# Kernel optimization log

Measured on AMD Instinct MI355X. Metric: run time of the kernel, lower is better.

The kernel has to match this reference:

```python
import jax, jax.numpy as jnp
import numpy as np

N_STATE = 1024
N_HEAD = 16
B = 2
S = 2048


def setup_inputs() -> dict:
    key = jax.random.key(0)
    ks = jax.random.split(key, 8)
    s = 0.02
    x = jax.random.normal(ks[0], (B, S, N_STATE), dtype=jnp.float32)
    # causal additive mask, as in Whisper: upper triangle = -inf
    mask = jnp.where(jnp.triu(jnp.ones((S, S), dtype=bool), k=1), -jnp.inf, 0.0).astype(jnp.float32)
    Wq = jax.random.normal(ks[1], (N_STATE, N_STATE), dtype=jnp.float32) * s
    bq = jax.random.normal(ks[2], (N_STATE,), dtype=jnp.float32) * s
    Wk = jax.random.normal(ks[3], (N_STATE, N_STATE), dtype=jnp.float32) * s
    Wv = jax.random.normal(ks[4], (N_STATE, N_STATE), dtype=jnp.float32) * s
    bv = jax.random.normal(ks[5], (N_STATE,), dtype=jnp.float32) * s
    Wo = jax.random.normal(ks[6], (N_STATE, N_STATE), dtype=jnp.float32) * s
    bo = jax.random.normal(ks[7], (N_STATE,), dtype=jnp.float32) * s
    return {"x": x, "mask": mask, "Wq": Wq, "bq": bq, "Wk": Wk,
            "Wv": Wv, "bv": bv, "Wo": Wo, "bo": bo}


def reference(x, mask, Wq, bq, Wk, Wv, bv, Wo, bo):
    Bb, S_, D = x.shape
    H = N_HEAD
    hd = D // H
    scale = hd ** (-0.25)  # scale split across q and k, as in the source
    q = x @ Wq.T + bq              # [B,S,D]
    k = x @ Wk.T                   # key has no bias
    v = x @ Wv.T + bv
    # [B,S,D] -> [B,H,S,hd]
    q = q.reshape(Bb, S_, H, hd).transpose(0, 2, 1, 3) * scale
    k = k.reshape(Bb, S_, H, hd).transpose(0, 2, 1, 3) * scale
    v = v.reshape(Bb, S_, H, hd).transpose(0, 2, 1, 3)
    qk = jnp.einsum('bhsd,bhtd->bhst', q, k) + mask[:S_, :S_]
    w = jax.nn.softmax(qk, axis=-1).astype(q.dtype)
    out = jnp.einsum('bhst,bhtd->bhsd', w, v)
    out = out.transpose(0, 2, 1, 3).reshape(Bb, S_, D)
    return out @ Wo.T + bo
```

## Files before the change

kernel.cpp:

```cpp
#include <hip/hip_runtime.h>
#include <hip/hip_bf16.h>
#include <cmath>

typedef __bf16 bf16;
typedef __bf16 bf16x8 __attribute__((ext_vector_type(8)));
typedef __bf16 bf16x4 __attribute__((ext_vector_type(4)));
typedef float f32x4 __attribute__((ext_vector_type(4)));

#define QS 0.18033688f

__device__ __forceinline__ void load16_to_lds(const void* g, void* l) {
    __builtin_amdgcn_global_load_lds(
        (const __attribute__((address_space(1))) unsigned int*)g,
        (__attribute__((address_space(3))) unsigned int*)l, 16, 0, 0);
}

__global__ __launch_bounds__(256) void convert_kernel(
    const float* __restrict__ x,  const float* __restrict__ wq,
    const float* __restrict__ wk, const float* __restrict__ wv,
    const float* __restrict__ wo, bf16* __restrict__ dst)
{
    const size_t M1 = 1024ull * 1024ull, M4 = 4ull * M1;
    size_t i0 = ((size_t)blockIdx.x * 256 + threadIdx.x) * 8;
    const float* s;
    size_t off;
    float sc = 1.f;
    if      (i0 < M4)        { s = x;  off = i0; }
    else if (i0 < M4 + M1)   { s = wq; off = i0 - M4; sc = QS; }
    else if (i0 < M4 + 2*M1) { s = wk; off = i0 - M4 - M1; }
    else if (i0 < M4 + 3*M1) { s = wv; off = i0 - M4 - 2*M1; }
    else                     { s = wo; off = i0 - M4 - 3*M1; }
    float4 a = *(const float4*)(s + off);
    float4 b = *(const float4*)(s + off + 4);
    bf16x8 r = { (bf16)(a.x*sc), (bf16)(a.y*sc), (bf16)(a.z*sc), (bf16)(a.w*sc),
                 (bf16)(b.x*sc), (bf16)(b.y*sc), (bf16)(b.z*sc), (bf16)(b.w*sc) };
    *(bf16x8*)(dst + i0) = r;
}

template<int BM, bool OUT_F32>
__device__ __forceinline__ void gemm_core(
    const bf16* __restrict__ A, const bf16* __restrict__ W,
    const float* __restrict__ bias, void* __restrict__ C,
    int mb, int nb, bool vt_out, float bias_scale)
{
    constexpr int IF = BM / 32;
    __shared__ __align__(16) bf16 As[BM * 32];
    __shared__ __align__(16) bf16 Bs[128 * 32];

    const int tid  = threadIdx.x;
    const int lane = tid & 63;
    const int wave = tid >> 6;
    const int wr   = (wave >> 1) * (BM / 2);
    const int wc   = (wave & 1) * 64;
    const int l15  = lane & 15;
    const int l4   = lane >> 4;
    const int swz  = (l4 ^ ((l15 >> 1) & 3)) * 8;

    f32x4 acc[IF][4] = {};

    for (int kt = 0; kt < 32; ++kt) {
#pragma unroll
        for (int it = 0; it < BM / 64; ++it) {
            int c = it * 256 + tid;
            int scol = ((c & 3) ^ ((c >> 3) & 3)) * 8;
            load16_to_lds(&A[(size_t)(mb * BM + (c >> 2)) * 1024 + kt * 32 + scol],
                          &As[(it * 256 + (tid & 192)) * 8]);
        }
#pragma unroll
        for (int it = 0; it < 2; ++it) {
            int c = it * 256 + tid;
            int scol = ((c & 3) ^ ((c >> 3) & 3)) * 8;
            load16_to_lds(&W[(size_t)(nb * 128 + (c >> 2)) * 1024 + kt * 32 + scol],
                          &Bs[(it * 256 + (tid & 192)) * 8]);
        }
        __syncthreads();
        bf16x8 af[IF], bfr[4];
#pragma unroll
        for (int i = 0; i < IF; ++i)
            af[i] = *(const bf16x8*)&As[(wr + i * 16 + l15) * 32 + swz];
#pragma unroll
        for (int j = 0; j < 4; ++j)
            bfr[j] = *(const bf16x8*)&Bs[(wc + j * 16 + l15) * 32 + swz];
#pragma unroll
        for (int i = 0; i < IF; ++i)
#pragma unroll
            for (int j = 0; j < 4; ++j)
                acc[i][j] = __builtin_amdgcn_mfma_f32_16x16x32_bf16(
                    af[i], bfr[j], acc[i][j], 0, 0, 0);
        __syncthreads();
    }

    if (!OUT_F32 && vt_out) {
#pragma unroll
        for (int j = 0; j < 4; ++j) {
            int col = nb * 128 + wc + j * 16 + l15;
            float bv = bias ? bias[col] : 0.f;
            int h = col >> 6, d = col & 63;
#pragma unroll
            for (int i = 0; i < IF; ++i) {
                int m0 = mb * BM + wr + i * 16 + l4 * 4;
                int b = m0 >> 11, s = m0 & 2047;
                bf16x4 pk = { (bf16)(acc[i][j][0] + bv), (bf16)(acc[i][j][1] + bv),
                              (bf16)(acc[i][j][2] + bv), (bf16)(acc[i][j][3] + bv) };
                *(bf16x4*)&((bf16*)C)[(size_t)((b * 16 + h) * 64 + d) * 2048 + s] = pk;
            }
        }
    } else {
#pragma unroll
        for (int j = 0; j < 4; ++j) {
            int col = nb * 128 + wc + j * 16 + l15;
            float bv = bias ? bias[col] * bias_scale : 0.f;
#pragma unroll
            for (int i = 0; i < IF; ++i) {
                int row0 = mb * BM + wr + i * 16 + l4 * 4;
#pragma unroll
                for (int r = 0; r < 4; ++r) {
                    float val = acc[i][j][r] + bv;
                    size_t idx = (size_t)(row0 + r) * 1024 + col;
                    if (OUT_F32) ((float*)C)[idx] = val;
                    else         ((bf16*)C)[idx]  = (bf16)val;
                }
            }
        }
    }
}

__global__ __launch_bounds__(256) void qkv_kernel(
    const bf16* __restrict__ xb,
    const bf16* __restrict__ wqb, const float* __restrict__ bq,
    const bf16* __restrict__ wkb,
    const bf16* __restrict__ wvb, const float* __restrict__ bv,
    bf16* __restrict__ q, bf16* __restrict__ k, bf16* __restrict__ vt)
{
    int mb = blockIdx.x;
    int nbg = blockIdx.y;
    int sel = nbg >> 3, nb = nbg & 7;
    const bf16* W = (sel == 0) ? wqb : ((sel == 1) ? wkb : wvb);
    const float* bias = (sel == 0) ? bq : ((sel == 2) ? bv : nullptr);
    bf16* C = (sel == 0) ? q : ((sel == 1) ? k : vt);
    gemm_core<128, false>(xb, W, bias, C, mb, nb, sel == 2,
                          sel == 0 ? QS : 1.f);
}

__global__ __launch_bounds__(256) void oproj_kernel(
    const bf16* __restrict__ ao, const bf16* __restrict__ wob,
    const float* __restrict__ bo, float* __restrict__ out)
{
    gemm_core<64, true>(ao, wob, bo, out, blockIdx.x, blockIdx.y, false, 1.f);
}

__global__ __launch_bounds__(256) void attn_kernel(
    const bf16* __restrict__ q, const bf16* __restrict__ k,
    const bf16* __restrict__ vt, bf16* __restrict__ o)
{
    __shared__ __align__(16) bf16 Ks[2][64 * 64];
    __shared__ __align__(16) bf16 Vs[2][64 * 64];
    __shared__ __align__(16) bf16 Ps[4][16 * 72];

    const int tid  = threadIdx.x;
    const int lane = tid & 63;
    const int wave = tid >> 6;
    const int l15  = lane & 15;
    const int l4   = lane >> 4;

    const int bh = blockIdx.x;
    const int pairIdx = blockIdx.y;
    const int b = bh >> 4, h = bh & 15;
    const int qts[2] = { pairIdx, 31 - pairIdx };

    auto stage = [&](int nt, int buf) {
#pragma unroll
        for (int it = 0; it < 2; ++it) {
            int c = it * 256 + tid;
            int scol = ((c & 7) ^ ((c >> 3) & 7)) * 8;
            load16_to_lds(&k[(size_t)(b * 2048 + nt * 64 + (c >> 3)) * 1024 + h * 64 + scol],
                          &Ks[buf][(it * 256 + (tid & 192)) * 8]);
            load16_to_lds(&vt[(size_t)(bh * 64 + (c >> 3)) * 2048 + nt * 64 + scol],
                          &Vs[buf][(it * 256 + (tid & 192)) * 8]);
        }
    };

    int b0 = 0;
    stage(0, 0);

    for (int seg = 0; seg < 2; ++seg) {
        const int qt = qts[seg];
        const int qg = qt * 64 + wave * 16 + l15;
        bf16x8 qf[2];
#pragma unroll
        for (int kk = 0; kk < 2; ++kk)
            qf[kk] = *(const bf16x8*)&q[(size_t)(b * 2048 + qg) * 1024 + h * 64 + kk * 32 + l4 * 8];

        f32x4 oacc[4] = {};
        float lsum = 0.f;

        const int n = qt + 1;
        for (int nt = 0; nt < n; ++nt) {
            __syncthreads();
            if (nt + 1 < n)      stage(nt + 1, b0 ^ 1);
            else if (seg == 0)   stage(0, b0 ^ 1);

            f32x4 s[4] = {};
#pragma unroll
            for (int kk = 0; kk < 2; ++kk) {
#pragma unroll
                for (int j = 0; j < 4; ++j) {
                    bf16x8 kf = *(const bf16x8*)&Ks[b0][(j * 16 + l15) * 64
                                    + (((kk * 4 + l4) ^ (l15 & 7)) * 8)];
                    s[j] = __builtin_amdgcn_mfma_f32_16x16x32_bf16(kf, qf[kk], s[j], 0, 0, 0);
                }
            }

            float pv[4][4];
            if (nt == qt) {
#pragma unroll
                for (int j = 0; j < 4; ++j)
#pragma unroll
                    for (int r = 0; r < 4; ++r) {
                        int kg = nt * 64 + j * 16 + l4 * 4 + r;
                        pv[j][r] = (kg > qg) ? 0.f : __builtin_amdgcn_exp2f(s[j][r]);
                    }
            } else {
#pragma unroll
                for (int j = 0; j < 4; ++j)
#pragma unroll
                    for (int r = 0; r < 4; ++r)
                        pv[j][r] = __builtin_amdgcn_exp2f(s[j][r]);
            }
#pragma unroll
            for (int j = 0; j < 4; ++j)
                lsum += (pv[j][0] + pv[j][1]) + (pv[j][2] + pv[j][3]);

#pragma unroll
            for (int j = 0; j < 4; ++j) {
                bf16x4 pk = { (bf16)pv[j][0], (bf16)pv[j][1], (bf16)pv[j][2], (bf16)pv[j][3] };
                *(bf16x4*)&Ps[wave][l15 * 72 + j * 16 + l4 * 4] = pk;
            }

#pragma unroll
            for (int kk = 0; kk < 2; ++kk) {
                bf16x8 pf = *(const bf16x8*)&Ps[wave][l15 * 72 + kk * 32 + l4 * 8];
#pragma unroll
                for (int f = 0; f < 4; ++f) {
                    bf16x8 vf = *(const bf16x8*)&Vs[b0][(f * 16 + l15) * 64
                                    + (((kk * 4 + l4) ^ (l15 & 7)) * 8)];
                    oacc[f] = __builtin_amdgcn_mfma_f32_16x16x32_bf16(pf, vf, oacc[f], 0, 0, 0);
                }
            }
            b0 ^= 1;
        }

        lsum += __shfl_xor(lsum, 16, 64);
        lsum += __shfl_xor(lsum, 32, 64);
        float rinv[4];
#pragma unroll
        for (int r = 0; r < 4; ++r) rinv[r] = 1.f / __shfl(lsum, l4 * 4 + r, 64);
#pragma unroll
        for (int f = 0; f < 4; ++f)
#pragma unroll
            for (int r = 0; r < 4; ++r)
                o[(size_t)(b * 2048 + qt * 64 + wave * 16 + l4 * 4 + r) * 1024 + h * 64 + f * 16 + l15]
                    = (bf16)(oacc[f][r] * rinv[r]);
    }
}

extern "C" void kernel_launch(void* const* d_in, const int* in_sizes, int n_in,
                              void* d_out, int out_size, void* d_ws, size_t ws_size,
                              hipStream_t stream)
{
    const float* x  = (const float*)d_in[0];
    const float* Wq = (const float*)d_in[2];
    const float* bq = (const float*)d_in[3];
    const float* Wk = (const float*)d_in[4];
    const float* Wv = (const float*)d_in[5];
    const float* bv = (const float*)d_in[6];
    const float* Wo = (const float*)d_in[7];
    const float* bo = (const float*)d_in[8];
    float* out = (float*)d_out;

    const size_t M1 = 1024ull * 1024ull, M4 = 4ull * M1;
    bf16* base = (bf16*)d_ws;
    bf16* xb  = base;
    bf16* wqb = base + M4;
    bf16* wkb = base + M4 + M1;
    bf16* wvb = base + M4 + 2 * M1;
    bf16* wob = base + M4 + 3 * M1;
    bf16* q   = base + 8 * M1;
    bf16* k   = base + 12 * M1;
    bf16* vt  = base + 16 * M1;
    bf16* ao  = xb;

    convert_kernel<<<4096, 256, 0, stream>>>(x, Wq, Wk, Wv, Wo, base);
    qkv_kernel<<<dim3(32, 24), 256, 0, stream>>>(xb, wqb, bq, wkb, wvb, bv, q, k, vt);
    attn_kernel<<<dim3(32, 16), 256, 0, stream>>>(q, k, vt, ao);
    oproj_kernel<<<dim3(64, 8), 256, 0, stream>>>(ao, wob, bo, out);
}
```

Before: 184.4 us.

## Process 128-row query tiles per attention block and enlarge o-proj GEMM tile

Each attention wave now handles two 16-row query sub-tiles (32 rows), so a block covers 128 query rows and reuses every staged K/V tile for twice as many queries. The grid shrinks to 8 balanced causal pairs per head, and waves skip key tiles that lie entirely above their rows. The output projection also switches to the 128-row GEMM tile with half the row blocks. This lowers K/V LDS staging and global traffic per query, at the cost of more registers, fewer blocks, and waves idling at barriers on skipped tiles.

```diff
diff --git a/kernel.cpp b/kernel.cpp
--- a/kernel.cpp
+++ b/kernel.cpp
@@ -146,7 +146,7 @@
     const bf16* __restrict__ ao, const bf16* __restrict__ wob,
     const float* __restrict__ bo, float* __restrict__ out)
 {
-    gemm_core<64, true>(ao, wob, bo, out, blockIdx.x, blockIdx.y, false, 1.f);
+    gemm_core<128, true>(ao, wob, bo, out, blockIdx.x, blockIdx.y, false, 1.f);
 }
 
 __global__ __launch_bounds__(256) void attn_kernel(
@@ -155,7 +155,7 @@
 {
     __shared__ __align__(16) bf16 Ks[2][64 * 64];
     __shared__ __align__(16) bf16 Vs[2][64 * 64];
-    __shared__ __align__(16) bf16 Ps[4][16 * 72];
+    __shared__ __align__(16) bf16 Ps[4][32 * 72];
 
     const int tid  = threadIdx.x;
     const int lane = tid & 63;
@@ -166,7 +166,7 @@
     const int bh = blockIdx.x;
     const int pairIdx = blockIdx.y;
     const int b = bh >> 4, h = bh & 15;
-    const int qts[2] = { pairIdx, 31 - pairIdx };
+    const int qts[2] = { pairIdx, 15 - pairIdx };
 
     auto stage = [&](int nt, int buf) {
 #pragma unroll
@@ -185,82 +185,99 @@
 
     for (int seg = 0; seg < 2; ++seg) {
         const int qt = qts[seg];
-        const int qg = qt * 64 + wave * 16 + l15;
-        bf16x8 qf[2];
-#pragma unroll
-        for (int kk = 0; kk < 2; ++kk)
-            qf[kk] = *(const bf16x8*)&q[(size_t)(b * 2048 + qg) * 1024 + h * 64 + kk * 32 + l4 * 8];
-
-        f32x4 oacc[4] = {};
-        float lsum = 0.f;
-
-        const int n = qt + 1;
+        const int qrow0 = qt * 128 + wave * 32;
+        bf16x8 qf[2][2];
+#pragma unroll
+        for (int qb = 0; qb < 2; ++qb)
+#pragma unroll
+            for (int kk = 0; kk < 2; ++kk)
+                qf[qb][kk] = *(const bf16x8*)&q[(size_t)(b * 2048 + qrow0 + qb * 16 + l15) * 1024
+                                               + h * 64 + kk * 32 + l4 * 8];
+
+        f32x4 oacc[2][4] = {};
+        float lsum[2] = { 0.f, 0.f };
+
+        const int n = 2 * qt + 2;
         for (int nt = 0; nt < n; ++nt) {
             __syncthreads();
             if (nt + 1 < n)      stage(nt + 1, b0 ^ 1);
             else if (seg == 0)   stage(0, b0 ^ 1);
 
-            f32x4 s[4] = {};
+            if (nt * 64 > qrow0 + 31) { b0 ^= 1; continue; }
+
+            f32x4 s[2][4] = {};
 #pragma unroll
             for (int kk = 0; kk < 2; ++kk) {
 #pragma unroll
                 for (int j = 0; j < 4; ++j) {
                     bf16x8 kf = *(const bf16x8*)&Ks[b0][(j * 16 + l15) * 64
                                     + (((kk * 4 + l4) ^ (l15 & 7)) * 8)];
-                    s[j] = __builtin_amdgcn_mfma_f32_16x16x32_bf16(kf, qf[kk], s[j], 0, 0, 0);
-                }
-            }
-
-            float pv[4][4];
-            if (nt == qt) {
+                    s[0][j] = __builtin_amdgcn_mfma_f32_16x16x32_bf16(kf, qf[0][kk], s[0][j], 0, 0, 0);
+                    s[1][j] = __builtin_amdgcn_mfma_f32_16x16x32_bf16(kf, qf[1][kk], s[1][j], 0, 0, 0);
+                }
+            }
+
+            const bool diag = (nt >= 2 * qt);
+#pragma unroll
+            for (int qb = 0; qb < 2; ++qb) {
+                float pv[4][4];
+                if (diag) {
+                    int qg = qrow0 + qb * 16 + l15;
+#pragma unroll
+                    for (int j = 0; j < 4; ++j)
+#pragma unroll
+                        for (int r = 0; r < 4; ++r) {
+                            int kg = nt * 64 + j * 16 + l4 * 4 + r;
+                            pv[j][r] = (kg > qg) ? 0.f : __builtin_amdgcn_exp2f(s[qb][j][r]);
+                        }
+                } else {
+#pragma unroll
+                    for (int j = 0; j < 4; ++j)
+#pragma unroll
+                        for (int r = 0; r < 4; ++r)
+                            pv[j][r] = __builtin_amdgcn_exp2f(s[qb][j][r]);
+                }
 #pragma unroll
                 for (int j = 0; j < 4; ++j)
-#pragma unroll
-                    for (int r = 0; r < 4; ++r) {
-                        int kg = nt * 64 + j * 16 + l4 * 4 + r;
-                        pv[j][r] = (kg > qg) ? 0.f : __builtin_amdgcn_exp2f(s[j][r]);
-                    }
-            } else {
-#pragma unroll
-                for (int j = 0; j < 4; ++j)
-#pragma unroll
-                    for (int r = 0; r < 4; ++r)
-                        pv[j][r] = __builtin_amdgcn_exp2f(s[j][r]);
-            }
-#pragma unroll
-            for (int j = 0; j < 4; ++j)
-                lsum += (pv[j][0] + pv[j][1]) + (pv[j][2] + pv[j][3]);
-
-#pragma unroll
-            for (int j = 0; j < 4; ++j) {
-                bf16x4 pk = { (bf16)pv[j][0], (bf16)pv[j][1], (bf16)pv[j][2], (bf16)pv[j][3] };
-                *(bf16x4*)&Ps[wave][l15 * 72 + j * 16 + l4 * 4] = pk;
+                    lsum[qb] += (pv[j][0] + pv[j][1]) + (pv[j][2] + pv[j][3]);
+
+#pragma unroll
+                for (int j = 0; j < 4; ++j) {
+                    bf16x4 pk = { (bf16)pv[j][0], (bf16)pv[j][1], (bf16)pv[j][2], (bf16)pv[j][3] };
+                    *(bf16x4*)&Ps[wave][(qb * 16 + l15) * 72 + j * 16 + l4 * 4] = pk;
+                }
             }
 
 #pragma unroll
             for (int kk = 0; kk < 2; ++kk) {
-                bf16x8 pf = *(const bf16x8*)&Ps[wave][l15 * 72 + kk * 32 + l4 * 8];
+                bf16x8 pf0 = *(const bf16x8*)&Ps[wave][l15 * 72 + kk * 32 + l4 * 8];
+                bf16x8 pf1 = *(const bf16x8*)&Ps[wave][(16 + l15) * 72 + kk * 32 + l4 * 8];
 #pragma unroll
                 for (int f = 0; f < 4; ++f) {
                     bf16x8 vf = *(const bf16x8*)&Vs[b0][(f * 16 + l15) * 64
                                     + (((kk * 4 + l4) ^ (l15 & 7)) * 8)];
-                    oacc[f] = __builtin_amdgcn_mfma_f32_16x16x32_bf16(pf, vf, oacc[f], 0, 0, 0);
+                    oacc[0][f] = __builtin_amdgcn_mfma_f32_16x16x32_bf16(pf0, vf, oacc[0][f], 0, 0, 0);
+                    oacc[1][f] = __builtin_amdgcn_mfma_f32_16x16x32_bf16(pf1, vf, oacc[1][f], 0, 0, 0);
                 }
             }
             b0 ^= 1;
         }
 
-        lsum += __shfl_xor(lsum, 16, 64);
-        lsum += __shfl_xor(lsum, 32, 64);
-        float rinv[4];
-#pragma unroll
-        for (int r = 0; r < 4; ++r) rinv[r] = 1.f / __shfl(lsum, l4 * 4 + r, 64);
-#pragma unroll
-        for (int f = 0; f < 4; ++f)
-#pragma unroll
-            for (int r = 0; r < 4; ++r)
-                o[(size_t)(b * 2048 + qt * 64 + wave * 16 + l4 * 4 + r) * 1024 + h * 64 + f * 16 + l15]
-                    = (bf16)(oacc[f][r] * rinv[r]);
+#pragma unroll
+        for (int qb = 0; qb < 2; ++qb) {
+            float ls = lsum[qb];
+            ls += __shfl_xor(ls, 16, 64);
+            ls += __shfl_xor(ls, 32, 64);
+            float rinv[4];
+#pragma unroll
+            for (int r = 0; r < 4; ++r) rinv[r] = 1.f / __shfl(ls, l4 * 4 + r, 64);
+#pragma unroll
+            for (int f = 0; f < 4; ++f)
+#pragma unroll
+                for (int r = 0; r < 4; ++r)
+                    o[(size_t)(b * 2048 + qrow0 + qb * 16 + l4 * 4 + r) * 1024 + h * 64 + f * 16 + l15]
+                        = (bf16)(oacc[qb][f][r] * rinv[r]);
+        }
     }
 }
 
@@ -292,6 +309,6 @@
 
     convert_kernel<<<4096, 256, 0, stream>>>(x, Wq, Wk, Wv, Wo, base);
     qkv_kernel<<<dim3(32, 24), 256, 0, stream>>>(xb, wqb, bq, wkb, wvb, bv, q, k, vt);
-    attn_kernel<<<dim3(32, 16), 256, 0, stream>>>(q, k, vt, ao);
-    oproj_kernel<<<dim3(64, 8), 256, 0, stream>>>(ao, wob, bo, out);
-}
+    attn_kernel<<<dim3(32, 8), 256, 0, stream>>>(q, k, vt, ao);
+    oproj_kernel<<<dim3(32, 8), 256, 0, stream>>>(ao, wob, bo, out);
+}
```

Result: slower. 199.7 us (+8.3%).
